# Kernel optimization log

Measured on AMD Instinct MI355X. Metric: run time of the kernel, lower is better.

Reference implementation:

```python
import jax, jax.numpy as jnp
import numpy as np

B, C, H, W = 4, 768, 64, 64
NC_PRED = 200   # classes in preds/text (!= 171 to trigger retrieval path)
NC_MEM = 171    # memory/text_coco classes
TC = 256        # transform_channels
OC = 768        # out_channels
BN_EPS = 1e-5


def setup_inputs() -> dict:
    key = jax.random.key(0)
    ks = jax.random.split(key, 32)
    n = lambda k, s, sc=1.0: jax.random.normal(k, s, jnp.float32) * sc
    g = lambda k, c: 1.0 + 0.1 * jax.random.normal(k, (c,), jnp.float32)
    inp = {
        'feats': n(ks[0], (B, C, H, W)),
        'preds': n(ks[1], (B, NC_PRED, H, W)),
        'text': n(ks[2], (1, NC_PRED, 1, C)),
        'memory': n(ks[3], (NC_MEM, 1, C)),      # self.memory buffer
        'text_mem': n(ks[4], (NC_MEM, 1, C)),    # self.text buffer
        # query_project: two 1x1 conv + BN + ReLU
        'qw1': n(ks[5], (TC, C), C ** -0.5), 'qg1': g(ks[6], TC), 'qb1': n(ks[7], (TC,), 0.1),
        'qw2': n(ks[8], (TC, TC), TC ** -0.5), 'qg2': g(ks[9], TC), 'qb2': n(ks[10], (TC,), 0.1),
        # key_project: two 1x1 conv + BN + ReLU
        'kw1': n(ks[11], (TC, C), C ** -0.5), 'kg1': g(ks[12], TC), 'kb1': n(ks[13], (TC,), 0.1),
        'kw2': n(ks[14], (TC, TC), TC ** -0.5), 'kg2': g(ks[15], TC), 'kb2': n(ks[16], (TC,), 0.1),
        # value_project: 1x1 conv + BN + ReLU
        'vw': n(ks[17], (TC, C), C ** -0.5), 'vg': g(ks[18], TC), 'vb': n(ks[19], (TC,), 0.1),
        # out_project: 1x1 conv + BN + ReLU (TC -> C)
        'ow': n(ks[20], (C, TC), TC ** -0.5), 'og': g(ks[21], C), 'ob': n(ks[22], (C,), 0.1),
        # bottleneck: 3x3 conv (2C -> OC) + BN + ReLU
        'bw': n(ks[23], (OC, 2 * C, 3, 3), (2 * C * 9) ** -0.5), 'bg': g(ks[24], OC), 'bb': n(ks[25], (OC,), 0.1),
    }
    return inp


def _cbr(x, w, gamma, beta):
    # 1x1 conv (no bias) + eval-mode BN (mean=0, var=1) + ReLU
    y = jnp.einsum('oc,bchw->bohw', w, x)
    s = (gamma / jnp.sqrt(1.0 + BN_EPS))[None, :, None, None]
    return jax.nn.relu(y * s + beta[None, :, None, None])


def _forward(feats, preds, text, memory, text_mem,
             qw1, qg1, qb1, qw2, qg2, qb2,
             kw1, kg1, kb1, kw2, kg2, kb2,
             vw, vg, vb, ow, og, ob, bw, bg, bb):
    b, c, h, w = feats.shape
    nc = preds.shape[1]
    # softmax class weights per pixel: [B*H*W, NC]
    wcls = jax.nn.softmax(preds.transpose(0, 2, 3, 1).reshape(-1, nc), axis=-1)
    # --- retrieval: cosine sim + argmax + gather (nc != 171 branch) ---
    t = text[0, :, 0, :]          # [NC_PRED, C]
    tc = text_mem[:, 0, :]        # [NC_MEM, C]
    mem = memory[:, 0, :]         # [NC_MEM, C]
    den = jnp.linalg.norm(t, axis=1)[:, None] * jnp.linalg.norm(tc, axis=1)[None, :]
    sim = (t @ tc.T) / jnp.maximum(den, 1e-8)
    idx = jnp.argmax(sim, axis=1)            # [NC_PRED]
    D = mem[idx]                             # gathered memory rows [NC_PRED, C]
    # soft aggregation
    sel = (wcls @ D).reshape(b, h, w, c).transpose(0, 3, 1, 2)  # [B,C,H,W]
    # --- self-attention: query=feats, key/value=selected memory ---
    q = _cbr(_cbr(feats, qw1, qg1, qb1), qw2, qg2, qb2).reshape(b, TC, h * w).transpose(0, 2, 1)  # [B,HW,TC]
    k = _cbr(_cbr(sel, kw1, kg1, kb1), kw2, kg2, kb2).reshape(b, TC, h * w)                        # [B,TC,HW]
    v = _cbr(sel, vw, vg, vb).reshape(b, TC, h * w).transpose(0, 2, 1)                             # [B,HW,TC]
    att = jax.nn.softmax(jnp.einsum('bqc,bck->bqk', q, k) * (TC ** -0.5), axis=-1)                 # [B,HW,HW]
    ctx = jnp.einsum('bqk,bkc->bqc', att, v).transpose(0, 2, 1).reshape(b, TC, h, w)
    sel_out = _cbr(ctx, ow, og, ob)          # [B,C,H,W]
    # --- bottleneck: 3x3 conv + BN + ReLU on concat ---
    x = jnp.concatenate([feats, sel_out], axis=1)
    y = jax.lax.conv_general_dilated(x, bw, (1, 1), 'SAME',
                                     dimension_numbers=('NCHW', 'OIHW', 'NCHW'))
    s = (bg / jnp.sqrt(1.0 + BN_EPS))[None, :, None, None]
    return jax.nn.relu(y * s + bb[None, :, None, None])


def reference(feats, preds, text, memory, text_mem,
              qw1, qg1, qb1, qw2, qg2, qb2,
              kw1, kg1, kb1, kw2, kg2, kb2,
              vw, vg, vb, ow, og, ob, bw, bg, bb):
    return _forward(feats, preds, text, memory, text_mem,
                    qw1, qg1, qb1, qw2, qg2, qb2,
                    kw1, kg1, kb1, kw2, kg2, kb2,
                    vw, vg, vb, ow, og, ob, bw, bg, bb)
```

## Files before the change

### kernel.cpp

```cpp
#include <hip/hip_runtime.h>
#include <stdint.h>

typedef unsigned short u16;
typedef __attribute__((ext_vector_type(8))) short short8;
typedef __attribute__((ext_vector_type(4))) float f32x4;

#define RSQC 0.9999950000374997f
#define OUT_ELEMS 12582912

__device__ __forceinline__ float bf2f(u16 u) {
  union { uint32_t i; float f; } v; v.i = ((uint32_t)u) << 16; return v.f;
}
__device__ __forceinline__ u16 f2bf(float f) {
  union { uint32_t i; float f; } v; v.f = f;
  uint32_t i = v.i;
  i += 0x7fffu + ((i >> 16) & 1u);
  return (u16)(i >> 16);
}
__device__ __forceinline__ void gload16(const u16* g, u16* l) {
  __builtin_amdgcn_global_load_lds(
      (const __attribute__((address_space(1))) uint32_t*)g,
      (__attribute__((address_space(3))) uint32_t*)l, 16, 0, 0);
}

__global__ __launch_bounds__(256) void probe_fill(float* out, float val) {
  for (size_t i = (size_t)blockIdx.x * 256 + threadIdx.x; i < OUT_ELEMS; i += (size_t)gridDim.x * 256)
    out[i] = val;
}


__global__ __launch_bounds__(64) void sim_argmax(const float* __restrict__ text,
                                                 const float* __restrict__ tmem,
                                                 int* __restrict__ idx) {
  const int i = blockIdx.x, lane = threadIdx.x;
  const float* t = text + (size_t)i * 768;
  float tr[12];
  float nt = 0.f;
#pragma unroll
  for (int k = 0; k < 12; ++k) { tr[k] = t[lane + k * 64]; nt += tr[k] * tr[k]; }
#pragma unroll
  for (int m = 32; m; m >>= 1) nt += __shfl_xor(nt, m);
  nt = sqrtf(nt);
  float best = -1e30f; int bj = 0;
  for (int j = 0; j < 171; ++j) {
    const float* tc = tmem + (size_t)j * 768;
    float dot = 0.f, nc = 0.f;
#pragma unroll
    for (int k = 0; k < 12; ++k) {
      float y = tc[lane + k * 64];
      dot += tr[k] * y;
      nc += y * y;
    }
#pragma unroll
    for (int m = 32; m; m >>= 1) {
      dot += __shfl_xor(dot, m);
      nc += __shfl_xor(nc, m);
    }
    float s = dot / fmaxf(nt * sqrtf(nc), 1e-8f);
    if (s > best) { best = s; bj = j; }
  }
  if (lane == 0) idx[i] = bj;
}

__global__ __launch_bounds__(256) void build_d(const float* __restrict__ memory,
                                               const int* __restrict__ idx,
                                               u16* __restrict__ D) {
  int i = blockIdx.x * 256 + threadIdx.x;
  if (i >= 256 * 768) return;
  int c = i % 768, j = i / 768;
  u16 v = 0;
  if (j < 200) {
    int ii = idx[j];
    ii = ii < 0 ? 0 : (ii > 170 ? 170 : ii);
    v = f2bf(memory[(size_t)ii * 768 + c]);
  }
  D[i] = v;
}

__global__ __launch_bounds__(256) void wcls_kernel(const float* __restrict__ preds,
                                                   u16* __restrict__ wcls) {
  __shared__ float red[4][64];
  const int tid = threadIdx.x;
  const int p = tid & 63, q = tid >> 6;
  const int pos = blockIdx.x * 64 + p;
  const int b = pos >> 12, hw = pos & 4095;
  const float* pp = preds + (size_t)b * 200 * 4096 + hw;
  const int nlo = q * 50, nhi = nlo + 50;
  float mx = -1e30f;
  for (int n = nlo; n < nhi; ++n) mx = fmaxf(mx, pp[(size_t)n * 4096]);
  red[q][p] = mx;
  __syncthreads();
  const float m = fmaxf(fmaxf(red[0][p], red[1][p]), fmaxf(red[2][p], red[3][p]));
  __syncthreads();
  float s = 0.f;
  for (int n = nlo; n < nhi; ++n) s += __expf(pp[(size_t)n * 4096] - m);
  red[q][p] = s;
  __syncthreads();
  const float inv = 1.f / (red[0][p] + red[1][p] + red[2][p] + red[3][p]);
  u16* w = wcls + (size_t)pos * 256;
#pragma unroll
  for (int c8 = 0; c8 < 8; ++c8) {
    short8 v;
    const int base = q * 64 + c8 * 8;
#pragma unroll
    for (int j = 0; j < 8; ++j) {
      const int n = base + j;
      float e = (n < 200) ? __expf(pp[(size_t)n * 4096] - m) * inv : 0.f;
      v[j] = (short)f2bf(e);
    }
    *(short8*)&w[base] = v;
  }
}

__global__ __launch_bounds__(256) void transpose_feats(const float* __restrict__ feats,
                                                       u16* __restrict__ ft) {
  __shared__ u16 t[64][65];
  const int bz = blockIdx.z, c0 = blockIdx.y * 64, p0 = blockIdx.x * 64;
  const int col = threadIdx.x & 63, row4 = threadIdx.x >> 6;
  const float* src = feats + ((size_t)bz * 768 + c0) * 4096 + p0;
#pragma unroll
  for (int i = 0; i < 16; ++i) {
    int ci = i * 4 + row4;
    t[ci][col] = f2bf(src[(size_t)ci * 4096 + col]);
  }
  __syncthreads();
  u16* dst = ft + ((size_t)bz * 4096 + p0) * 768 + c0;
#pragma unroll
  for (int i = 0; i < 16; ++i) {
    int pi = i * 4 + row4;
    dst[(size_t)pi * 768 + col] = t[col][pi];
  }
}

__global__ __launch_bounds__(256) void cast_all(
    const float* __restrict__ s0, u16* __restrict__ d0,
    const float* __restrict__ s1, u16* __restrict__ d1,
    const float* __restrict__ s2, u16* __restrict__ d2,
    const float* __restrict__ s3, u16* __restrict__ d3,
    const float* __restrict__ s4, u16* __restrict__ d4,
    const float* __restrict__ s5, u16* __restrict__ d5) {
  int i = blockIdx.x * 256 + threadIdx.x;
  if (i < 196608) d0[i] = f2bf(s0[i]);
  else if (i < 393216) d1[i - 196608] = f2bf(s1[i - 196608]);
  else if (i < 589824) d2[i - 393216] = f2bf(s2[i - 393216]);
  else if (i < 786432) d3[i - 589824] = f2bf(s3[i - 589824]);
  else if (i < 851968) d4[i - 786432] = f2bf(s4[i - 786432]);
  else if (i < 917504) d5[i - 851968] = f2bf(s5[i - 851968]);
}

__global__ __launch_bounds__(256) void repack2(const float* __restrict__ bw,
                                               u16* __restrict__ w9f, int c_base) {
  const int gid = blockIdx.x * 4 + (threadIdx.x >> 6);
  const int lane = threadIdx.x & 63;
  const int mfrag = gid % 48, kc = gid / 48;
  const int o = mfrag * 16 + (lane & 15);
  const int c = c_base + kc * 32 + (lane >> 4) * 8;
  const float* src = bw + ((size_t)o * 1536 + c) * 9;
  float v[72];
#pragma unroll
  for (int t = 0; t < 72; ++t) v[t] = src[t];
#pragma unroll
  for (int tap = 0; tap < 9; ++tap) {
    short8 w;
#pragma unroll
    for (int j = 0; j < 8; ++j) w[j] = (short)f2bf(v[j * 9 + tap]);
    *(short8*)&w9f[(((size_t)(kc * 9 + tap) * 48 + mfrag) << 9) + lane * 8] = w;
  }
}

template <bool EP>
__global__ __launch_bounds__(256) void gemm_std(
    const u16* __restrict__ A, const u16* __restrict__ Bt, u16* __restrict__ out,
    const float* __restrict__ g, const float* __restrict__ bia,
    int N, int K, int lda, int ldb) {
  __shared__ __attribute__((aligned(16))) u16 As[2][128 * 32];
  __shared__ __attribute__((aligned(16))) u16 Bs[2][128 * 32];
  const int tid = threadIdx.x, lane = tid & 63, wv = tid >> 6;
  const int wr = wv >> 1, wc = wv & 1;
  const int m0 = blockIdx.y * 128, n0 = blockIdx.x * 128;
  const int r0 = lane >> 2, ksl = (lane & 3) * 8;
  const int wofs = (lane >> 2) * 32 + (((lane & 3) ^ ((lane >> 3) & 3)) << 3);
  const int rsl = (((lane >> 4) ^ ((lane >> 1) & 3)) << 3);
  f32x4 acc[4][4] = {};
  const int nt = K >> 5;

  short8 a0[2], b0[2], a1[2], b1[2];
  auto LOAD = [&](int t, short8 av[2], short8 bv[2]) {
    const int k0 = t << 5;
#pragma unroll
    for (int i = 0; i < 2; ++i) {
      const int row = (wv * 2 + i) * 16 + r0;
      av[i] = *(const short8*)(A + (size_t)(m0 + row) * lda + k0 + ksl);
      bv[i] = *(const short8*)(Bt + (size_t)(n0 + row) * ldb + k0 + ksl);
    }
  };
  auto STORE = [&](int buf, short8 av[2], short8 bv[2]) {
#pragma unroll
    for (int i = 0; i < 2; ++i) {
      const int o = (wv * 2 + i) * 512 + wofs;
      *(short8*)&As[buf][o] = av[i];
      *(short8*)&Bs[buf][o] = bv[i];
    }
  };
  auto COMPUTE = [&](int buf) {
    short8 a[4], b[4];
#pragma unroll
    for (int mi = 0; mi < 4; ++mi)
      a[mi] = *(const short8*)&As[buf][(wr * 4 + mi) * 512 + (lane & 15) * 32 + rsl];
#pragma unroll
    for (int ni = 0; ni < 4; ++ni)
      b[ni] = *(const short8*)&Bs[buf][(wc * 4 + ni) * 512 + (lane & 15) * 32 + rsl];
#pragma unroll
    for (int mi = 0; mi < 4; ++mi)
#pragma unroll
      for (int ni = 0; ni < 4; ++ni)
        acc[mi][ni] = __builtin_amdgcn_mfma_f32_16x16x32_bf16(a[mi], b[ni], acc[mi][ni], 0, 0, 0);
  };

  LOAD(0, a0, b0);
  for (int t = 0; t < nt; t += 2) {
    STORE(0, a0, b0);
    __syncthreads();
    LOAD(t + 1, a1, b1);
    COMPUTE(0);
    STORE(1, a1, b1);
    __syncthreads();
    if (t + 2 < nt) LOAD(t + 2, a0, b0);
    COMPUTE(1);
  }
  const int mb = m0 + wr * 64 + ((lane >> 4) << 2);
  const int nb = n0 + wc * 64 + (lane & 15);
#pragma unroll
  for (int ni = 0; ni < 4; ++ni) {
    const int n = nb + ni * 16;
    float s = 1.f, bb_ = 0.f;
    if (EP) { s = g[n] * RSQC; bb_ = bia[n]; }
#pragma unroll
    for (int mi = 0; mi < 4; ++mi)
#pragma unroll
      for (int r = 0; r < 4; ++r) {
        float v = acc[mi][ni][r];
        if (EP) v = fmaxf(v * s + bb_, 0.f);
        out[(size_t)(mb + mi * 16 + r) * N + n] = f2bf(v);
      }
  }
}

__global__ __launch_bounds__(256) void gemm_swv(
    const u16* __restrict__ A, const u16* __restrict__ Bt, u16* __restrict__ out,
    const float* __restrict__ g, const float* __restrict__ bia,
    int Mtot, int K, int lda, int ldb) {
  __shared__ __attribute__((aligned(16))) u16 As[2][128 * 32];
  __shared__ __attribute__((aligned(16))) u16 Bs[2][128 * 32];
  const int tid = threadIdx.x, lane = tid & 63, wv = tid >> 6;
  const int wr = wv >> 1, wc = wv & 1;
  const int m0 = blockIdx.y * 128, n0 = blockIdx.x * 128;
  const int r0 = lane >> 2, ksl = (lane & 3) * 8;
  const int wofs = (lane >> 2) * 32 + (((lane & 3) ^ ((lane >> 3) & 3)) << 3);
  const int rsl = (((lane >> 4) ^ ((lane >> 1) & 3)) << 3);
  f32x4 acc[4][4] = {};
  const int nt = K >> 5;

  short8 a0[2], b0[2], a1[2], b1[2];
  auto LOAD = [&](int t, short8 av[2], short8 bv[2]) {
    const int k0 = t << 5;
#pragma unroll
    for (int i = 0; i < 2; ++i) {
      const int row = (wv * 2 + i) * 16 + r0;
      av[i] = *(const short8*)(A + (size_t)(m0 + row) * lda + k0 + ksl);
      bv[i] = *(const short8*)(Bt + (size_t)(n0 + row) * ldb + k0 + ksl);
    }
  };
  auto STORE = [&](int buf, short8 av[2], short8 bv[2]) {
#pragma unroll
    for (int i = 0; i < 2; ++i) {
      const int o = (wv * 2 + i) * 512 + wofs;
      *(short8*)&As[buf][o] = av[i];
      *(short8*)&Bs[buf][o] = bv[i];
    }
  };
  auto COMPUTE = [&](int buf) {
    short8 a[4], b[4];
#pragma unroll
    for (int mi = 0; mi < 4; ++mi)
      a[mi] = *(const short8*)&As[buf][(wr * 4 + mi) * 512 + (lane & 15) * 32 + rsl];
#pragma unroll
    for (int ni = 0; ni < 4; ++ni)
      b[ni] = *(const short8*)&Bs[buf][(wc * 4 + ni) * 512 + (lane & 15) * 32 + rsl];
#pragma unroll
    for (int mi = 0; mi < 4; ++mi)
#pragma unroll
      for (int ni = 0; ni < 4; ++ni)
        acc[mi][ni] = __builtin_amdgcn_mfma_f32_16x16x32_bf16(a[mi], b[ni], acc[mi][ni], 0, 0, 0);
  };

  LOAD(0, a0, b0);
  for (int t = 0; t < nt; t += 2) {
    STORE(0, a0, b0);
    __syncthreads();
    LOAD(t + 1, a1, b1);
    COMPUTE(0);
    STORE(1, a1, b1);
    __syncthreads();
    if (t + 2 < nt) LOAD(t + 2, a0, b0);
    COMPUTE(1);
  }
  const int mb = m0 + wr * 64 + ((lane >> 4) << 2);
  const int nb = n0 + wc * 64 + (lane & 15);
#pragma unroll
  for (int mi = 0; mi < 4; ++mi)
#pragma unroll
    for (int r = 0; r < 4; ++r) {
      const int m = mb + mi * 16 + r;
      const float s = g[m] * RSQC, bb_ = bia[m];
#pragma unroll
      for (int ni = 0; ni < 4; ++ni) {
        const int n = nb + ni * 16;
        out[((size_t)(n >> 12) * Mtot + m) * 4096 + (n & 4095)] =
            f2bf(fmaxf(acc[mi][ni][r] * s + bb_, 0.f));
      }
    }
}

template <int MODE>
__global__ __launch_bounds__(256) void conv_frag(
    const u16* __restrict__ Af, const u16* __restrict__ X, float* out,
    const float* __restrict__ g, const float* __restrict__ bia) {
  __shared__ __attribute__((aligned(16))) u16 Hb[2][264 * 32];
  const int tid = threadIdx.x, lane = tid & 63, wv = tid >> 6;
  const int wr = wv >> 1, wc = wv & 1;
  const int id = blockIdx.y * 128 + blockIdx.x;
  const int xcd = id & 7, sl = id >> 3;
  const int m0 = (sl % 6) * 128;
  const int n0 = (xcd * 16 + sl / 6) * 128;
  f32x4 acc[4][4] = {};

  int vmask[4];
#pragma unroll
  for (int i = 0; i < 4; ++i) {
    const int hw = (n0 + wc * 64 + i * 16 + (lane & 15)) & 4095;
    const int h = hw >> 6, w = hw & 63;
    int m = 0;
#pragma unroll
    for (int t = 0; t < 9; ++t)
      if ((unsigned)(h + t / 3 - 1) < 64u && (unsigned)(w + t % 3 - 1) < 64u) m |= 1 << t;
    vmask[i] = m;
  }

  const int fb = (m0 >> 4) + wr * 4;
  auto aload = [&](int kc, int tap, short8 d[4]) {
    const u16* base = Af + ((size_t)((kc * 9 + tap) * 48 + fb) << 9) + lane * 8;
#pragma unroll
    for (int mi = 0; mi < 4; ++mi) d[mi] = *(const short8*)(base + (mi << 9));
  };
  auto hstage = [&](int kc, int buf) {
#pragma unroll
    for (int j = 0; j < 5; ++j) {
      const int cid = tid + j * 256;
      if (cid < 1032) {
        int q = n0 - 65 + (cid >> 2);
        q = q < 0 ? 0 : (q > 16383 ? 16383 : q);
        const int row = cid >> 2;
        const int s = (cid & 3) ^ ((row >> 1) & 3);
        gload16(X + (size_t)q * 768 + kc * 32 + s * 8, &Hb[buf][(size_t)cid * 8]);
      }
    }
  };

  hstage(0, 0);
  short8 acur[4], anxt[4];
  aload(0, 0, acur);
  __syncthreads();
  int p = 0;
  for (int kc = 0; kc < 24; ++kc) {
    if (kc < 23) hstage(kc + 1, p ^ 1);
#pragma unroll
    for (int tap = 0; tap < 9; ++tap) {
      const int nk = (tap == 8) ? (kc == 23 ? 23 : kc + 1) : kc;
      const int ntp = (tap == 8) ? 0 : tap + 1;
      aload(nk, ntp, anxt);
      const int shift = (tap / 3 - 1) * 64 + (tap % 3 - 1);
#pragma unroll
      for (int ni = 0; ni < 4; ++ni) {
        const int hrow = wc * 64 + ni * 16 + (lane & 15) + 65 + shift;
        short8 bv = *(const short8*)((const char*)&Hb[p][0] + hrow * 64 +
                                     (((lane >> 4) ^ ((hrow >> 1) & 3)) << 4));
        short8 z = {};
        if (!((vmask[ni] >> tap) & 1)) bv = z;
#pragma unroll
        for (int mi = 0; mi < 4; ++mi)
          acc[mi][ni] = __builtin_amdgcn_mfma_f32_16x16x32_bf16(acur[mi], bv, acc[mi][ni], 0, 0, 0);
      }
#pragma unroll
      for (int mi = 0; mi < 4; ++mi) acur[mi] = anxt[mi];
    }
    if (kc < 23) {
      __syncthreads();
      p ^= 1;
    }
  }
  const int mb = m0 + wr * 64 + ((lane >> 4) << 2);
  const int nb = n0 + wc * 64 + (lane & 15);
#pragma unroll
  for (int mi = 0; mi < 4; ++mi)
#pragma unroll
    for (int r = 0; r < 4; ++r) {
      const int m = mb + mi * 16 + r;
      float s = 0.f, bb_ = 0.f;
      if (MODE == 2) { s = g[m] * RSQC; bb_ = bia[m]; }
#pragma unroll
      for (int ni = 0; ni < 4; ++ni) {
        const int n = nb + ni * 16;
        const size_t oidx = ((size_t)(n >> 12) * 768 + m) * 4096 + (n & 4095);
        if (MODE == 1) out[oidx] = acc[mi][ni][r];
        else out[oidx] = fmaxf((acc[mi][ni][r] + out[oidx]) * s + bb_, 0.f);
      }
    }
}

__global__ __launch_bounds__(256) void flash_attn(const u16* Q,
                                                  const u16* __restrict__ Kg,
                                                  const u16* __restrict__ Vt,
                                                  u16* ctx) {
  __shared__ __attribute__((aligned(16))) u16 KVs[64 * 256];
  __shared__ __attribute__((aligned(16))) u16 Ps[4096];
  const int tid = threadIdx.x, lane = tid & 63, wv = tid >> 6;
  const int b = blockIdx.y, q0 = blockIdx.x * 64;
  const u16* qb = Q + ((size_t)b * 4096 + q0) * 256;
  const u16* kb = Kg + (size_t)b * 4096 * 256;
  const u16* vb = Vt + (size_t)b * 256 * 4096;
  const float scale = 0.0625f;

  short8 qf[8];
  {
    const int arow = wv * 16 + (lane & 15);
    const u16* qrow = qb + (size_t)arow * 256 + (lane >> 4) * 8;
#pragma unroll
    for (int kk = 0; kk < 8; ++kk) qf[kk] = *(const short8*)(qrow + kk * 32);
  }
  float mreg[4] = {-1e30f, -1e30f, -1e30f, -1e30f};
  float lsum[4] = {0.f, 0.f, 0.f, 0.f};
  f32x4 o[16] = {};

  for (int t = 0; t < 64; ++t) {
    {
      const int r = tid >> 5, sb = (tid & 31) * 16;
      const char* ksrc = (const char*)(kb + (size_t)t * 64 * 256);
#pragma unroll
      for (int i = 0; i < 8; ++i) {
        int row = i * 8 + r;
        short8 v = *(const short8*)(ksrc + (size_t)row * 512 + sb);
        *(short8*)((char*)KVs + row * 512 + (sb ^ ((row & 7) << 4))) = v;
      }
    }
    __syncthreads();
    f32x4 s4[4] = {};
    __builtin_amdgcn_s_setprio(1);
#pragma unroll
    for (int kk = 0; kk < 8; ++kk) {
      const int cb = (kk * 32 + ((lane >> 4) * 8)) * 2;
#pragma unroll
      for (int ni = 0; ni < 4; ++ni) {
        const int brow = ni * 16 + (lane & 15);
        short8 bb = *(const short8*)((const char*)KVs + brow * 512 + (cb ^ ((brow & 7) << 4)));
        s4[ni] = __builtin_amdgcn_mfma_f32_16x16x32_bf16(qf[kk], bb, s4[ni], 0, 0, 0);
      }
    }
    __builtin_amdgcn_s_setprio(0);
    float al[4], p[4][4];
#pragma unroll
    for (int r = 0; r < 4; ++r) {
      float v0 = fmaxf(fmaxf(s4[0][r], s4[1][r]), fmaxf(s4[2][r], s4[3][r]));
      v0 = fmaxf(v0, __shfl_xor(v0, 1));
      v0 = fmaxf(v0, __shfl_xor(v0, 2));
      v0 = fmaxf(v0, __shfl_xor(v0, 4));
      v0 = fmaxf(v0, __shfl_xor(v0, 8));
      const float mn = fmaxf(mreg[r], v0 * scale);
      al[r] = __expf(mreg[r] - mn);
      mreg[r] = mn;
      float srow = 0.f;
#pragma unroll
      for (int ni = 0; ni < 4; ++ni) {
        float pv = __expf(s4[ni][r] * scale - mn);
        p[ni][r] = pv;
        srow += pv;
      }
      srow += __shfl_xor(srow, 1);
      srow += __shfl_xor(srow, 2);
      srow += __shfl_xor(srow, 4);
      srow += __shfl_xor(srow, 8);
      lsum[r] = lsum[r] * al[r] + srow;
    }
#pragma unroll
    for (int nf = 0; nf < 16; ++nf)
#pragma unroll
      for (int r = 0; r < 4; ++r) o[nf][r] *= al[r];
    {
      char* pbase = (char*)Ps + wv * 2048;
#pragma unroll
      for (int ni = 0; ni < 4; ++ni)
#pragma unroll
        for (int r = 0; r < 4; ++r) {
          const int row = ((lane >> 4) << 2) + r, col = ni * 16 + (lane & 15);
          *(u16*)(pbase + row * 128 + ((col * 2) ^ ((row & 7) << 4))) = f2bf(p[ni][r]);
        }
    }
    __syncthreads();
    {
      const int slot = tid & 7;
#pragma unroll
      for (int i = 0; i < 8; ++i) {
        const int cc = i * 32 + (tid >> 3);
        short8 v = *(const short8*)((const char*)vb + ((size_t)cc * 4096 + t * 64) * 2 + slot * 16);
        *(short8*)((char*)KVs + cc * 128 + ((slot * 16) ^ ((cc & 7) << 4))) = v;
      }
    }
    __syncthreads();
    short8 pa[2];
#pragma unroll
    for (int kk = 0; kk < 2; ++kk) {
      const int row = lane & 15;
      const int cb = (kk * 32 + ((lane >> 4) * 8)) * 2;
      pa[kk] = *(const short8*)((const char*)Ps + wv * 2048 + row * 128 + (cb ^ ((row & 7) << 4)));
    }
    __builtin_amdgcn_s_setprio(1);
#pragma unroll
    for (int nf = 0; nf < 16; ++nf) {
      const int crow = nf * 16 + (lane & 15);
#pragma unroll
      for (int kk = 0; kk < 2; ++kk) {
        const int kb2 = (kk * 32 + ((lane >> 4) * 8)) * 2;
        short8 bb = *(const short8*)((const char*)KVs + crow * 128 + (kb2 ^ ((crow & 7) << 4)));
        o[nf] = __builtin_amdgcn_mfma_f32_16x16x32_bf16(pa[kk], bb, o[nf], 0, 0, 0);
      }
    }
    __builtin_amdgcn_s_setprio(0);
    __syncthreads();
  }
  u16* cb_ = ctx + ((size_t)b * 4096 + q0) * 256;
#pragma unroll
  for (int r = 0; r < 4; ++r) {
    const int row = wv * 16 + ((lane >> 4) << 2) + r;
    const float inv = 1.f / lsum[r];
#pragma unroll
    for (int nf = 0; nf < 16; ++nf) {
      const int col = nf * 16 + (lane & 15);
      cb_[(size_t)row * 256 + col] = f2bf(o[nf][r] * inv);
    }
  }
}


extern "C" void kernel_launch(void* const* d_in, const int* in_sizes, int n_in,
                              void* d_out, int out_size, void* d_ws, size_t ws_size,
                              hipStream_t stream) {
  (void)in_sizes; (void)n_in; (void)out_size;
  const float* feats  = (const float*)d_in[0];
  const float* preds  = (const float*)d_in[1];
  const float* text   = (const float*)d_in[2];
  const float* memory = (const float*)d_in[3];
  const float* tmem   = (const float*)d_in[4];
  const float* qw1 = (const float*)d_in[5];  const float* qg1 = (const float*)d_in[6];  const float* qb1 = (const float*)d_in[7];
  const float* qw2 = (const float*)d_in[8];  const float* qg2 = (const float*)d_in[9];  const float* qb2 = (const float*)d_in[10];
  const float* kw1 = (const float*)d_in[11]; const float* kg1 = (const float*)d_in[12]; const float* kb1 = (const float*)d_in[13];
  const float* kw2 = (const float*)d_in[14]; const float* kg2 = (const float*)d_in[15]; const float* kb2 = (const float*)d_in[16];
  const float* vw  = (const float*)d_in[17]; const float* vg  = (const float*)d_in[18]; const float* vb  = (const float*)d_in[19];
  const float* ow  = (const float*)d_in[20]; const float* og  = (const float*)d_in[21]; const float* ob  = (const float*)d_in[22];
  const float* bw  = (const float*)d_in[23]; const float* bg  = (const float*)d_in[24]; const float* bb  = (const float*)d_in[25];

  float* dout = (float*)d_out;
  char* ws = (char*)d_ws;
  u16* featsT = (u16*)(ws);
  u16* selout = (u16*)(ws + 25165824);
  u16* S2     = (u16*)(ws + 50331648);
  u16* qw1c   = (u16*)(ws + 58720256);
  u16* kw1c   = (u16*)(ws + 59113472);
  u16* vwc    = (u16*)(ws + 59506688);
  u16* owc    = (u16*)(ws + 59899904);
  u16* qw2c   = (u16*)(ws + 60293120);
  u16* kw2c   = (u16*)(ws + 60424192);
  u16* w9     = S2;
  const size_t WS_NEED = 60948480;
  u16* D   = selout;
  u16* KD  = (u16*)((char*)selout + 393216);
  u16* VD  = (u16*)((char*)selout + 524288);
  int* idx = (int*)((char*)selout + 655360);
  u16* O0 = (u16*)dout;
  u16* O1 = O0 + 4194304;
  u16* O2 = O0 + 8388608;

  if (ws_size < WS_NEED) {
    probe_fill<<<2048, 256, 0, stream>>>(dout, 1000.0f);
    return;
  }

  u16* wcls = O0;
  u16* k1 = S2, *q1 = S2;
  u16* kbuf = O1, *vT = O2;
  u16* qbuf = O0, *ctx = O0;

  sim_argmax<<<200, 64, 0, stream>>>(text, tmem, idx);
  build_d<<<768, 256, 0, stream>>>(memory, idx, D);
  wcls_kernel<<<256, 256, 0, stream>>>(preds, wcls);
  transpose_feats<<<dim3(64, 12, 4), 256, 0, stream>>>(feats, featsT);
  cast_all<<<3584, 256, 0, stream>>>(qw1, qw1c, kw1, kw1c, vw, vwc, ow, owc, qw2, qw2c, kw2, kw2c);

  gemm_std<false><<<dim3(2, 2), 256, 0, stream>>>(kw1c, D, KD, nullptr, nullptr, 256, 768, 768, 768);
  gemm_std<false><<<dim3(2, 2), 256, 0, stream>>>(vwc, D, VD, nullptr, nullptr, 256, 768, 768, 768);

  gemm_std<true><<<dim3(2, 128), 256, 0, stream>>>(wcls, KD, k1, kg1, kb1, 256, 256, 256, 256);
  gemm_std<true><<<dim3(2, 128), 256, 0, stream>>>(k1, kw2c, kbuf, kg2, kb2, 256, 256, 256, 256);
  gemm_swv<<<dim3(128, 2), 256, 0, stream>>>(VD, wcls, vT, vg, vb, 256, 256, 256, 256);
  gemm_std<true><<<dim3(2, 128), 256, 0, stream>>>(featsT, qw1c, q1, qg1, qb1, 256, 768, 768, 768);
  gemm_std<true><<<dim3(2, 128), 256, 0, stream>>>(q1, qw2c, qbuf, qg2, qb2, 256, 256, 256, 256);
  flash_attn<<<dim3(64, 4), 256, 0, stream>>>(qbuf, kbuf, vT, ctx);
  gemm_std<true><<<dim3(6, 128), 256, 0, stream>>>(ctx, owc, selout, og, ob, 768, 256, 256, 256);
  repack2<<<288, 256, 0, stream>>>(bw, w9, 0);
  conv_frag<1><<<dim3(128, 6), 256, 0, stream>>>(w9, featsT, dout, nullptr, nullptr);
  repack2<<<288, 256, 0, stream>>>(bw, w9, 768);
  conv_frag<2><<<dim3(128, 6), 256, 0, stream>>>(w9, selout, dout, bg, bb);
}
```

Before: 834.3 us.

## Replace second-half conv with smaller-tile XCD-aware conv kernel

Adds a new conv_ms kernel for the second-half (selout) 3x3 conv. It uses 64x128 output tiles instead of the previous tile shape and launches 1536 blocks with an XCD-interleaved block-to-tile mapping. It double-buffers the input halo rows in LDS via global_load_lds and prefetches A fragments one tap ahead. The aim is more parallelism and better L2 locality per XCD, at the cost of less register reuse per block and more redundant halo loads.

After: 821.4 us, median of 2. About the same (-1.5%).

```diff
diff --git a/kernel.cpp b/kernel.cpp
--- a/kernel.cpp
+++ b/kernel.cpp
@@ -418,6 +418,99 @@
     }
 }
 
+__global__ __launch_bounds__(256) void conv_ms(
+    const u16* __restrict__ Af, const u16* __restrict__ X, float* out,
+    const float* __restrict__ g, const float* __restrict__ bia) {
+  __shared__ __attribute__((aligned(16))) u16 Hb[2][264 * 32];
+  const int tid = threadIdx.x, lane = tid & 63, wv = tid >> 6;
+  const int wr = wv >> 1, wc = wv & 1;
+  const int id = blockIdx.x;
+  const int xcd = id & 7, sl = id >> 3;
+  const int m0 = (sl % 12) * 64;
+  const int n0 = (xcd * 16 + sl / 12) * 128;
+  f32x4 acc[2][4] = {};
+
+  int vmask[4];
+#pragma unroll
+  for (int i = 0; i < 4; ++i) {
+    const int hw = (n0 + wc * 64 + i * 16 + (lane & 15)) & 4095;
+    const int h = hw >> 6, w = hw & 63;
+    int m = 0;
+#pragma unroll
+    for (int t = 0; t < 9; ++t)
+      if ((unsigned)(h + t / 3 - 1) < 64u && (unsigned)(w + t % 3 - 1) < 64u) m |= 1 << t;
+    vmask[i] = m;
+  }
+
+  const int fb = (m0 >> 4) + wr * 2;
+  auto aload = [&](int kc, int tap, short8 d[2]) {
+    const u16* base = Af + ((size_t)((kc * 9 + tap) * 48 + fb) << 9) + lane * 8;
+#pragma unroll
+    for (int mi = 0; mi < 2; ++mi) d[mi] = *(const short8*)(base + (mi << 9));
+  };
+  auto hstage = [&](int kc, int buf) {
+#pragma unroll
+    for (int j = 0; j < 5; ++j) {
+      const int cid = tid + j * 256;
+      if (cid < 1032) {
+        int q = n0 - 65 + (cid >> 2);
+        q = q < 0 ? 0 : (q > 16383 ? 16383 : q);
+        const int row = cid >> 2;
+        const int s = (cid & 3) ^ ((row >> 1) & 3);
+        gload16(X + (size_t)q * 768 + kc * 32 + s * 8, &Hb[buf][(size_t)cid * 8]);
+      }
+    }
+  };
+
+  hstage(0, 0);
+  short8 acur[2], anxt[2];
+  aload(0, 0, acur);
+  __syncthreads();
+  int p = 0;
+  for (int kc = 0; kc < 24; ++kc) {
+    if (kc < 23) hstage(kc + 1, p ^ 1);
+#pragma unroll
+    for (int tap = 0; tap < 9; ++tap) {
+      const int nk = (tap == 8) ? (kc == 23 ? 23 : kc + 1) : kc;
+      const int ntp = (tap == 8) ? 0 : tap + 1;
+      aload(nk, ntp, anxt);
+      const int shift = (tap / 3 - 1) * 64 + (tap % 3 - 1);
+#pragma unroll
+      for (int ni = 0; ni < 4; ++ni) {
+        const int hrow = wc * 64 + ni * 16 + (lane & 15) + 65 + shift;
+        short8 bv = *(const short8*)((const char*)&Hb[p][0] + hrow * 64 +
+                                     (((lane >> 4) ^ ((hrow >> 1) & 3)) << 4));
+        short8 z = {};
+        if (!((vmask[ni] >> tap) & 1)) bv = z;
+#pragma unroll
+        for (int mi = 0; mi < 2; ++mi)
+          acc[mi][ni] = __builtin_amdgcn_mfma_f32_16x16x32_bf16(acur[mi], bv, acc[mi][ni], 0, 0, 0);
+      }
+#pragma unroll
+      for (int mi = 0; mi < 2; ++mi) acur[mi] = anxt[mi];
+    }
+    if (kc < 23) {
+      __syncthreads();
+      p ^= 1;
+    }
+  }
+  const int mb = m0 + wr * 32 + ((lane >> 4) << 2);
+  const int nb = n0 + wc * 64 + (lane & 15);
+#pragma unroll
+  for (int mi = 0; mi < 2; ++mi)
+#pragma unroll
+    for (int r = 0; r < 4; ++r) {
+      const int m = mb + mi * 16 + r;
+      const float s = g[m] * RSQC, bb_ = bia[m];
+#pragma unroll
+      for (int ni = 0; ni < 4; ++ni) {
+        const int n = nb + ni * 16;
+        const size_t oidx = ((size_t)(n >> 12) * 768 + m) * 4096 + (n & 4095);
+        out[oidx] = fmaxf((acc[mi][ni][r] + out[oidx]) * s + bb_, 0.f);
+      }
+    }
+}
+
 __global__ __launch_bounds__(256) void flash_attn(const u16* Q,
                                                   const u16* __restrict__ Kg,
                                                   const u16* __restrict__ Vt,
@@ -618,5 +711,5 @@
   repack2<<<288, 256, 0, stream>>>(bw, w9, 0);
   conv_frag<1><<<dim3(128, 6), 256, 0, stream>>>(w9, featsT, dout, nullptr, nullptr);
   repack2<<<288, 256, 0, stream>>>(bw, w9, 768);
-  conv_frag<2><<<dim3(128, 6), 256, 0, stream>>>(w9, selout, dout, bg, bb);
-}
+  conv_ms<<<1536, 256, 0, stream>>>(w9, selout, dout, bg, bb);
+}
```
